# Performance work log

Measured on AMD Instinct MI355X. Metric: run time of the kernel, lower is better.

## Reference

```python
import jax, jax.numpy as jnp
import numpy as np

DIM = 256
NUM_HEADS = 8


def setup_inputs() -> dict:
    key = jax.random.key(0)
    ks = jax.random.split(key, 8)
    B, H, W = 2, 64, 64
    s = 0.02
    return {
        "query": jax.random.normal(ks[0], (B, H, W, DIM), jnp.float32),
        "sim": jax.random.normal(ks[1], (B, H, W, DIM), jnp.float32),
        "Wq": jax.random.normal(ks[2], (DIM, DIM), jnp.float32) * s,
        "bq": jnp.zeros((DIM,), jnp.float32),
        "Wkv": jax.random.normal(ks[3], (DIM, 2 * DIM), jnp.float32) * s,
        "bkv": jnp.zeros((2 * DIM,), jnp.float32),
        "Wp": jax.random.normal(ks[4], (DIM, DIM), jnp.float32) * s,
        "bp": jnp.zeros((DIM,), jnp.float32),
    }


def reference(query, sim, Wq, bq, Wkv, bkv, Wp, bp):
    B, H, W, dim = query.shape
    nh = NUM_HEADS
    dh = dim // nh
    scale = dh ** (-0.5)
    S = H * W

    # projections
    q = (query.reshape(B, S, dim) @ Wq + bq).reshape(B, S, nh, dh)
    kv = (sim.reshape(B, S, dim) @ Wkv + bkv).reshape(B, S, 2, nh, dh)
    k = kv[:, :, 0]  # [B,S,nh,dh]
    v = kv[:, :, 1]

    # attention: scores [B,nh,S,S]
    attn = jnp.einsum('bqhd,bkhd->bhqk', q * scale, k)
    attn = jax.nn.softmax(attn, axis=-1)
    x = jnp.einsum('bhqk,bkhd->bqhd', attn, v)  # [B,S,nh,dh]
    x = x.reshape(B, H, W, dim)
    return x @ Wp + bp
```

## Files before the change

kernel.cpp:

```cpp
#include <hip/hip_runtime.h>
#include <hip/hip_bf16.h>
#include <math.h>


#define SCALE 0.17677669529663687f
#define LOG2E 1.4426950408889634f

typedef __attribute__((ext_vector_type(8))) short short8;
typedef __attribute__((ext_vector_type(4))) float f32x4;

static __device__ __forceinline__ unsigned short f2bf(float x) {
    union { float f; unsigned int u; } v; v.f = x;
    unsigned int r = v.u + 0x7fff + ((v.u >> 16) & 1);
    return (unsigned short)(r >> 16);
}
static __device__ __forceinline__ float bf2f(unsigned short h) {
    union { unsigned int u; float f; } v; v.u = ((unsigned int)h) << 16;
    return v.f;
}
static __device__ __forceinline__ float fexp2(float x) {
#if __has_builtin(__builtin_amdgcn_exp2f)
    return __builtin_amdgcn_exp2f(x);
#else
    float r; asm("v_exp_f32 %0, %1" : "=v"(r) : "v"(x)); return r;
#endif
}
static __device__ __forceinline__ unsigned int pk_bf16(float a, float b) {
    unsigned int r;
    asm("v_cvt_pk_bf16_f32 %0, %1, %2" : "=v"(r) : "v"(a), "v"(b));
    return r;
}

__global__ __launch_bounds__(256) void prep_w(
    const float* __restrict__ Wq, const float* __restrict__ Wkv,
    const float* __restrict__ Wp,
    unsigned short* __restrict__ whi, unsigned short* __restrict__ wlo)
{
    const int n = blockIdx.x & 255, mat = blockIdx.x >> 8, k = threadIdx.x;
    const float* src; int ldw, colx; float sc = 1.f;
    if (mat == 0)      { src = Wq;  ldw = 256; colx = n;       sc = SCALE * LOG2E; }
    else if (mat == 1) { src = Wkv; ldw = 512; colx = n;       }
    else if (mat == 2) { src = Wkv; ldw = 512; colx = n + 256; }
    else               { src = Wp;  ldw = 256; colx = n;       }
    float v = src[(long long)k * ldw + colx] * sc;
    unsigned short h = f2bf(v);
    unsigned short l = f2bf(v - bf2f(h));
    const int o = blockIdx.x * 256 + k;
    whi[o] = h; wlo[o] = l;
}

__global__ __launch_bounds__(256) void gemm_qkv(
    const float* __restrict__ query, const float* __restrict__ sim,
    const unsigned short* __restrict__ whi, const unsigned short* __restrict__ wlo,
    const float* __restrict__ bq, const float* __restrict__ bkv,
    unsigned short* __restrict__ qbuf, unsigned short* __restrict__ kbuf,
    unsigned short* __restrict__ vTb)
{
    __shared__ unsigned short XsH[64 * 40], XsL[64 * 40];
    __shared__ unsigned short WsH[64 * 40], WsL[64 * 40];

    const int t = threadIdx.x, wave = t >> 6, lane = t & 63;
    const int col = lane & 15, quad = lane >> 4;
    const int by = blockIdx.y;
    const int kind = by >> 2;
    const int n0 = (by & 3) * 64;
    const int m0 = blockIdx.x * 64;
    const float* __restrict__ X = (kind == 0) ? query : sim;
    const int wrow0 = kind * 256 + n0;
    const int srow = t >> 2, spart = (t & 3) * 8;

    const f32x4 zero = {0.f, 0.f, 0.f, 0.f};
    f32x4 acc[4] = {zero, zero, zero, zero};

    for (int kt = 0; kt < 8; ++kt) {
        const int k0 = kt * 32;
        const float* xp = &X[(long long)(m0 + srow) * 256 + k0 + spart];
        float4 xa = *(const float4*)xp;
        float4 xb = *(const float4*)(xp + 4);
        float xv[8] = {xa.x, xa.y, xa.z, xa.w, xb.x, xb.y, xb.z, xb.w};
        union { unsigned short s[8]; uint4 u; } ph, pl;
#pragma unroll
        for (int j = 0; j < 8; ++j) {
            unsigned short h = f2bf(xv[j]);
            ph.s[j] = h;
            pl.s[j] = f2bf(xv[j] - bf2f(h));
        }
        uint4 wh = *(const uint4*)&whi[(long long)(wrow0 + srow) * 256 + k0 + spart];
        uint4 wl = *(const uint4*)&wlo[(long long)(wrow0 + srow) * 256 + k0 + spart];
        __syncthreads();
        *(uint4*)&XsH[srow * 40 + spart] = ph.u;
        *(uint4*)&XsL[srow * 40 + spart] = pl.u;
        *(uint4*)&WsH[srow * 40 + spart] = wh;
        *(uint4*)&WsL[srow * 40 + spart] = wl;
        __syncthreads();

        const unsigned short* Ah = (kind == 2) ? WsH : XsH;
        const unsigned short* Al = (kind == 2) ? WsL : XsL;
        const unsigned short* Bh = (kind == 2) ? XsH : WsH;
        const unsigned short* Bl = (kind == 2) ? XsL : WsL;

        short8 a_h = *(const short8*)(Ah + (wave * 16 + col) * 40 + quad * 8);
        short8 a_l = *(const short8*)(Al + (wave * 16 + col) * 40 + quad * 8);
#pragma unroll
        for (int nt = 0; nt < 4; ++nt) {
            short8 b_h = *(const short8*)(Bh + (nt * 16 + col) * 40 + quad * 8);
            short8 b_l = *(const short8*)(Bl + (nt * 16 + col) * 40 + quad * 8);
            acc[nt] = __builtin_amdgcn_mfma_f32_16x16x32_bf16(a_h, b_h, acc[nt], 0, 0, 0);
            acc[nt] = __builtin_amdgcn_mfma_f32_16x16x32_bf16(a_l, b_h, acc[nt], 0, 0, 0);
            acc[nt] = __builtin_amdgcn_mfma_f32_16x16x32_bf16(a_h, b_l, acc[nt], 0, 0, 0);
        }
    }

    if (kind == 0) {
#pragma unroll
        for (int nt = 0; nt < 4; ++nt) {
            int n = n0 + nt * 16 + col;
            int h = n >> 5, d = n & 31;
            float bias = bq[n] * (SCALE * LOG2E);
#pragma unroll
            for (int r = 0; r < 4; ++r) {
                int mg = m0 + wave * 16 + quad * 4 + r;
                int b = mg >> 12, sidx = mg & 4095;
                qbuf[((long long)(b * 8 + h) * 4096 + sidx) * 32 + d] = f2bf(acc[nt][r] + bias);
            }
        }
    } else if (kind == 1) {
#pragma unroll
        for (int nt = 0; nt < 4; ++nt) {
            int n = n0 + nt * 16 + col;
            int h = n >> 5, d = n & 31;
            float bias = bkv[n];
#pragma unroll
            for (int r = 0; r < 4; ++r) {
                int mg = m0 + wave * 16 + quad * 4 + r;
                int b = mg >> 12, sidx = mg & 4095;
                kbuf[((long long)(b * 8 + h) * 4096 + sidx) * 32 + d] = f2bf(acc[nt][r] + bias);
            }
        }
    } else {
#pragma unroll
        for (int nt = 0; nt < 4; ++nt) {
            int s = m0 + nt * 16 + col;
            int b = s >> 12, sidx = s & 4095;
#pragma unroll
            for (int r = 0; r < 4; ++r) {
                int dcol = n0 + wave * 16 + quad * 4 + r;
                int h = dcol >> 5, dd = dcol & 31;
                float bias = bkv[256 + dcol];
                vTb[((long long)((b * 8 + h) * 32 + dd)) * 4096 + sidx] = f2bf(acc[nt][r] + bias);
            }
        }
    }
}

__global__ __launch_bounds__(256) void flash_mfma(
    const unsigned short* __restrict__ qbuf,
    const unsigned short* __restrict__ kbuf,
    const unsigned short* __restrict__ vT,
    float* __restrict__ xbuf)
{
    __shared__ unsigned short Ks[128 * 40];
    __shared__ unsigned short Vt[32 * 136];
    __shared__ unsigned short Pb[4][640];

    const int t = threadIdx.x;
    const int wave = t >> 6, lane = t & 63;
    const int col = lane & 15, quad = lane >> 4;
    const int bh = blockIdx.x >> 5;
    const int q0 = (blockIdx.x & 31) * 128 + wave * 32;
    const long long kvbase = (long long)bh * 4096 * 32;
    unsigned short* pbw = Pb[wave];

    const short8 qf0 = *(const short8*)(qbuf + kvbase + (long long)(q0 + col) * 32 + quad * 8);
    const short8 qf1 = *(const short8*)(qbuf + kvbase + (long long)(q0 + 16 + col) * 32 + quad * 8);

    const f32x4 zero = {0.f, 0.f, 0.f, 0.f};
    f32x4 o00 = zero, o01 = zero, o10 = zero, o11 = zero;
    float l0 = 0.f, l1 = 0.f;

    const int krow = t >> 2, kpart = (t & 3) * 8;
    const int vrow = t >> 4, vpart = (t & 15) * 8;

    for (int kt = 0; kt < 32; ++kt) {
        uint4 kg0 = *(const uint4*)(kbuf + kvbase + (long long)(kt * 128 + krow) * 32 + kpart);
        uint4 kg1 = *(const uint4*)(kbuf + kvbase + (long long)(kt * 128 + krow + 64) * 32 + kpart);
        uint4 vg0 = *(const uint4*)(vT + ((long long)(bh * 32 + vrow)) * 4096 + kt * 128 + vpart);
        uint4 vg1 = *(const uint4*)(vT + ((long long)(bh * 32 + vrow + 16)) * 4096 + kt * 128 + vpart);
        __syncthreads();
        *(uint4*)(Ks + krow * 40 + kpart) = kg0;
        *(uint4*)(Ks + (krow + 64) * 40 + kpart) = kg1;
        *(uint4*)(Vt + vrow * 136 + vpart) = vg0;
        *(uint4*)(Vt + (vrow + 16) * 136 + vpart) = vg1;
        __syncthreads();

#pragma unroll
        for (int sb = 0; sb < 4; ++sb) {
            const int kb = sb * 32;
            short8 a0 = *(const short8*)(Ks + (kb + col) * 40 + quad * 8);
            short8 a1 = *(const short8*)(Ks + (kb + 16 + col) * 40 + quad * 8);
            short8 v0 = *(const short8*)(Vt + col * 136 + kb + quad * 8);
            short8 v1 = *(const short8*)(Vt + (16 + col) * 136 + kb + quad * 8);
            {
                f32x4 c0 = __builtin_amdgcn_mfma_f32_16x16x32_bf16(a0, qf0, zero, 0, 0, 0);
                f32x4 c1 = __builtin_amdgcn_mfma_f32_16x16x32_bf16(a1, qf0, zero, 0, 0, 0);
                float p0 = fexp2(c0[0]), p1 = fexp2(c0[1]), p2 = fexp2(c0[2]), p3 = fexp2(c0[3]);
                float p4 = fexp2(c1[0]), p5 = fexp2(c1[1]), p6 = fexp2(c1[2]), p7 = fexp2(c1[3]);
                l0 += ((p0 + p1) + (p2 + p3)) + ((p4 + p5) + (p6 + p7));
                uint2 w0 = make_uint2(pk_bf16(p0, p1), pk_bf16(p2, p3));
                uint2 w1 = make_uint2(pk_bf16(p4, p5), pk_bf16(p6, p7));
                *(uint2*)(pbw + col * 40 + quad * 4) = w0;
                *(uint2*)(pbw + col * 40 + 16 + quad * 4) = w1;
                short8 pf = *(const short8*)(pbw + col * 40 + quad * 8);
                o00 = __builtin_amdgcn_mfma_f32_16x16x32_bf16(v0, pf, o00, 0, 0, 0);
                o01 = __builtin_amdgcn_mfma_f32_16x16x32_bf16(v1, pf, o01, 0, 0, 0);
            }
            {
                f32x4 c0 = __builtin_amdgcn_mfma_f32_16x16x32_bf16(a0, qf1, zero, 0, 0, 0);
                f32x4 c1 = __builtin_amdgcn_mfma_f32_16x16x32_bf16(a1, qf1, zero, 0, 0, 0);
                float p0 = fexp2(c0[0]), p1 = fexp2(c0[1]), p2 = fexp2(c0[2]), p3 = fexp2(c0[3]);
                float p4 = fexp2(c1[0]), p5 = fexp2(c1[1]), p6 = fexp2(c1[2]), p7 = fexp2(c1[3]);
                l1 += ((p0 + p1) + (p2 + p3)) + ((p4 + p5) + (p6 + p7));
                uint2 w0 = make_uint2(pk_bf16(p0, p1), pk_bf16(p2, p3));
                uint2 w1 = make_uint2(pk_bf16(p4, p5), pk_bf16(p6, p7));
                *(uint2*)(pbw + col * 40 + quad * 4) = w0;
                *(uint2*)(pbw + col * 40 + 16 + quad * 4) = w1;
                short8 pf = *(const short8*)(pbw + col * 40 + quad * 8);
                o10 = __builtin_amdgcn_mfma_f32_16x16x32_bf16(v0, pf, o10, 0, 0, 0);
                o11 = __builtin_amdgcn_mfma_f32_16x16x32_bf16(v1, pf, o11, 0, 0, 0);
            }
        }
    }

    l0 += __shfl_xor(l0, 16, 64); l0 += __shfl_xor(l0, 32, 64);
    l1 += __shfl_xor(l1, 16, 64); l1 += __shfl_xor(l1, 32, 64);
    const float i0 = 1.f / l0, i1 = 1.f / l1;

    const int b = bh >> 3, hh = bh & 7;
    float* xp0 = xbuf + ((long long)(b * 4096 + q0 + col)) * 256 + hh * 32;
    *(float4*)(xp0 + quad * 4)      = make_float4(o00[0] * i0, o00[1] * i0, o00[2] * i0, o00[3] * i0);
    *(float4*)(xp0 + 16 + quad * 4) = make_float4(o01[0] * i0, o01[1] * i0, o01[2] * i0, o01[3] * i0);
    float* xp1 = xbuf + ((long long)(b * 4096 + q0 + 16 + col)) * 256 + hh * 32;
    *(float4*)(xp1 + quad * 4)      = make_float4(o10[0] * i1, o10[1] * i1, o10[2] * i1, o10[3] * i1);
    *(float4*)(xp1 + 16 + quad * 4) = make_float4(o11[0] * i1, o11[1] * i1, o11[2] * i1, o11[3] * i1);
}

__global__ __launch_bounds__(256) void gemm_outp(
    const float* __restrict__ xbuf,
    const unsigned short* __restrict__ whi, const unsigned short* __restrict__ wlo,
    const float* __restrict__ bp, float* __restrict__ out)
{
    __shared__ unsigned short XsH[64 * 40], XsL[64 * 40];
    __shared__ unsigned short WsH[64 * 40], WsL[64 * 40];

    const int t = threadIdx.x, wave = t >> 6, lane = t & 63;
    const int col = lane & 15, quad = lane >> 4;
    const int n0 = blockIdx.y * 64;
    const int m0 = blockIdx.x * 64;
    const int wrow0 = 768 + n0;
    const int srow = t >> 2, spart = (t & 3) * 8;

    const f32x4 zero = {0.f, 0.f, 0.f, 0.f};
    f32x4 acc[4] = {zero, zero, zero, zero};

    for (int kt = 0; kt < 8; ++kt) {
        const int k0 = kt * 32;
        const float* xp = &xbuf[(long long)(m0 + srow) * 256 + k0 + spart];
        float4 xa = *(const float4*)xp;
        float4 xb = *(const float4*)(xp + 4);
        float xv[8] = {xa.x, xa.y, xa.z, xa.w, xb.x, xb.y, xb.z, xb.w};
        union { unsigned short s[8]; uint4 u; } ph, pl;
#pragma unroll
        for (int j = 0; j < 8; ++j) {
            unsigned short h = f2bf(xv[j]);
            ph.s[j] = h;
            pl.s[j] = f2bf(xv[j] - bf2f(h));
        }
        uint4 wh = *(const uint4*)&whi[(long long)(wrow0 + srow) * 256 + k0 + spart];
        uint4 wl = *(const uint4*)&wlo[(long long)(wrow0 + srow) * 256 + k0 + spart];
        __syncthreads();
        *(uint4*)&XsH[srow * 40 + spart] = ph.u;
        *(uint4*)&XsL[srow * 40 + spart] = pl.u;
        *(uint4*)&WsH[srow * 40 + spart] = wh;
        *(uint4*)&WsL[srow * 40 + spart] = wl;
        __syncthreads();

        short8 a_h = *(const short8*)(XsH + (wave * 16 + col) * 40 + quad * 8);
        short8 a_l = *(const short8*)(XsL + (wave * 16 + col) * 40 + quad * 8);
#pragma unroll
        for (int nt = 0; nt < 4; ++nt) {
            short8 b_h = *(const short8*)(WsH + (nt * 16 + col) * 40 + quad * 8);
            short8 b_l = *(const short8*)(WsL + (nt * 16 + col) * 40 + quad * 8);
            acc[nt] = __builtin_amdgcn_mfma_f32_16x16x32_bf16(a_h, b_h, acc[nt], 0, 0, 0);
            acc[nt] = __builtin_amdgcn_mfma_f32_16x16x32_bf16(a_l, b_h, acc[nt], 0, 0, 0);
            acc[nt] = __builtin_amdgcn_mfma_f32_16x16x32_bf16(a_h, b_l, acc[nt], 0, 0, 0);
        }
    }

#pragma unroll
    for (int nt = 0; nt < 4; ++nt) {
        int n = n0 + nt * 16 + col;
        float bias = bp[n];
#pragma unroll
        for (int r = 0; r < 4; ++r) {
            int mg = m0 + wave * 16 + quad * 4 + r;
            out[(long long)mg * 256 + n] = acc[nt][r] + bias;
        }
    }
}

extern "C" void kernel_launch(void* const* d_in, const int* in_sizes, int n_in,
                              void* d_out, int out_size, void* d_ws, size_t ws_size,
                              hipStream_t stream) {
    const float* query = (const float*)d_in[0];
    const float* sim   = (const float*)d_in[1];
    const float* Wq    = (const float*)d_in[2];
    const float* bq    = (const float*)d_in[3];
    const float* Wkv   = (const float*)d_in[4];
    const float* bkv   = (const float*)d_in[5];
    const float* Wp    = (const float*)d_in[6];
    const float* bp    = (const float*)d_in[7];
    float* out = (float*)d_out;

    unsigned short* wsb = (unsigned short*)d_ws;
    unsigned short* qbuf = wsb;
    unsigned short* kbuf = wsb + 2097152;
    unsigned short* vT   = wsb + 4194304;
    float* xbuf = (float*)(wsb + 6291456);
    unsigned short* whi  = wsb + 10485760;
    unsigned short* wlo  = whi + 262144;

    prep_w   <<<dim3(1024),    256, 0, stream>>>(Wq, Wkv, Wp, whi, wlo);
    gemm_qkv <<<dim3(128, 12), 256, 0, stream>>>(query, sim, whi, wlo, bq, bkv,
                                                 qbuf, kbuf, vT);
    flash_mfma<<<dim3(512),    256, 0, stream>>>(qbuf, kbuf, vT, xbuf);
    gemm_outp<<<dim3(128, 4),  256, 0, stream>>>(xbuf, whi, wlo, bp, out);
}
```

Baseline: 176.1 us.

## Switch projection GEMMs to fp16 split-activation with single fp16 weights, prepack inputs

Replaces the bf16 hi/lo three-MFMA scheme with fp16: activations are split into fp16 hi/lo, weights are a single fp16 copy, and each tile needs two MFMAs instead of three. The prep kernel now pre-splits query/sim into fp16 hi/lo buffers and transposes the weights through shared memory for coalesced access. This cuts MFMA count and weight traffic in the GEMMs, but it adds a pass that writes and rereads the activations, and fp16 range and weight rounding may reduce accuracy. xbuf now aliases the xhi/xlo region, which is safe only because gemm_qkv finishes before flash writes it.

```diff
diff --git a/kernel.cpp b/kernel.cpp
--- a/kernel.cpp
+++ b/kernel.cpp
@@ -7,6 +7,7 @@
 #define LOG2E 1.4426950408889634f
 
 typedef __attribute__((ext_vector_type(8))) short short8;
+typedef __attribute__((ext_vector_type(8))) _Float16 half8;
 typedef __attribute__((ext_vector_type(4))) float f32x4;
 
 static __device__ __forceinline__ unsigned short f2bf(float x) {
@@ -30,34 +31,80 @@
     asm("v_cvt_pk_bf16_f32 %0, %1, %2" : "=v"(r) : "v"(a), "v"(b));
     return r;
 }
-
-__global__ __launch_bounds__(256) void prep_w(
+static __device__ __forceinline__ unsigned short f2h(float x) {
+    _Float16 h = (_Float16)x;
+    union { _Float16 h; unsigned short s; } u; u.h = h;
+    return u.s;
+}
+static __device__ __forceinline__ float h2f(unsigned short s) {
+    union { _Float16 h; unsigned short s; } u; u.s = s;
+    return (float)u.h;
+}
+
+__global__ __launch_bounds__(256) void prep(
+    const float* __restrict__ query, const float* __restrict__ sim,
     const float* __restrict__ Wq, const float* __restrict__ Wkv,
     const float* __restrict__ Wp,
-    unsigned short* __restrict__ whi, unsigned short* __restrict__ wlo)
+    unsigned short* __restrict__ xhi, unsigned short* __restrict__ xlo,
+    unsigned short* __restrict__ wfp)
 {
-    const int n = blockIdx.x & 255, mat = blockIdx.x >> 8, k = threadIdx.x;
-    const float* src; int ldw, colx; float sc = 1.f;
-    if (mat == 0)      { src = Wq;  ldw = 256; colx = n;       sc = SCALE * LOG2E; }
-    else if (mat == 1) { src = Wkv; ldw = 512; colx = n;       }
-    else if (mat == 2) { src = Wkv; ldw = 512; colx = n + 256; }
-    else               { src = Wp;  ldw = 256; colx = n;       }
-    float v = src[(long long)k * ldw + colx] * sc;
-    unsigned short h = f2bf(v);
-    unsigned short l = f2bf(v - bf2f(h));
-    const int o = blockIdx.x * 256 + k;
-    whi[o] = h; wlo[o] = l;
+    __shared__ float T[64][68];
+    const int blk = blockIdx.x, t = threadIdx.x;
+    if (blk < 4096) {
+        const int e = blk * 1024 + t * 4;
+        const float* src = (e < 2097152) ? (query + e) : (sim + (e - 2097152));
+        float4 v = *(const float4*)src;
+        float xv[4] = {v.x, v.y, v.z, v.w};
+        union { unsigned short s[4]; uint2 u; } ph, pl;
+#pragma unroll
+        for (int j = 0; j < 4; ++j) {
+            unsigned short h = f2h(xv[j]);
+            ph.s[j] = h;
+            pl.s[j] = f2h(xv[j] - h2f(h));
+        }
+        *(uint2*)&xhi[e] = ph.u;
+        *(uint2*)&xlo[e] = pl.u;
+        return;
+    }
+    const int bb = blk - 4096;
+    const int mat = bb >> 4, tile = bb & 15;
+    const int kr0 = (tile >> 2) * 64;
+    const int nc0 = (tile & 3) * 64;
+    const float* src; int ldw, cb; float sc = 1.f;
+    if (mat == 0)      { src = Wq;  ldw = 256; cb = 0;   sc = SCALE * LOG2E; }
+    else if (mat == 1) { src = Wkv; ldw = 512; cb = 0;   }
+    else if (mat == 2) { src = Wkv; ldw = 512; cb = 256; }
+    else               { src = Wp;  ldw = 256; cb = 0;   }
+    {
+        const int rl = t >> 4, c4 = (t & 15) * 4;
+#pragma unroll
+        for (int rr = 0; rr < 4; ++rr) {
+            float4 v = *(const float4*)&src[(long long)(kr0 + rr * 16 + rl) * ldw + cb + nc0 + c4];
+            T[rr * 16 + rl][c4 + 0] = v.x; T[rr * 16 + rl][c4 + 1] = v.y;
+            T[rr * 16 + rl][c4 + 2] = v.z; T[rr * 16 + rl][c4 + 3] = v.w;
+        }
+    }
+    __syncthreads();
+    {
+        const int nl = t >> 2, kl0 = (t & 3) * 16;
+        const long long orow = (long long)(mat * 256 + nc0 + nl) * 256 + kr0 + kl0;
+        union { unsigned short s[16]; uint4 u[2]; } ph;
+#pragma unroll
+        for (int j = 0; j < 16; ++j)
+            ph.s[j] = f2h(T[kl0 + j][nl] * sc);
+        *(uint4*)&wfp[orow] = ph.u[0];
+        *(uint4*)&wfp[orow + 8] = ph.u[1];
+    }
 }
 
 __global__ __launch_bounds__(256) void gemm_qkv(
-    const float* __restrict__ query, const float* __restrict__ sim,
-    const unsigned short* __restrict__ whi, const unsigned short* __restrict__ wlo,
+    const unsigned short* __restrict__ xhi, const unsigned short* __restrict__ xlo,
+    const unsigned short* __restrict__ wfp,
     const float* __restrict__ bq, const float* __restrict__ bkv,
     unsigned short* __restrict__ qbuf, unsigned short* __restrict__ kbuf,
     unsigned short* __restrict__ vTb)
 {
-    __shared__ unsigned short XsH[64 * 40], XsL[64 * 40];
-    __shared__ unsigned short WsH[64 * 40], WsL[64 * 40];
+    __shared__ unsigned short XsH[64 * 40], XsL[64 * 40], Ws[64 * 40];
 
     const int t = threadIdx.x, wave = t >> 6, lane = t & 63;
     const int col = lane & 15, quad = lane >> 4;
@@ -65,7 +112,7 @@
     const int kind = by >> 2;
     const int n0 = (by & 3) * 64;
     const int m0 = blockIdx.x * 64;
-    const float* __restrict__ X = (kind == 0) ? query : sim;
+    const int xrow0 = ((kind == 0) ? 0 : 8192) + m0;
     const int wrow0 = kind * 256 + n0;
     const int srow = t >> 2, spart = (t & 3) * 8;
 
@@ -74,40 +121,33 @@
 
     for (int kt = 0; kt < 8; ++kt) {
         const int k0 = kt * 32;
-        const float* xp = &X[(long long)(m0 + srow) * 256 + k0 + spart];
-        float4 xa = *(const float4*)xp;
-        float4 xb = *(const float4*)(xp + 4);
-        float xv[8] = {xa.x, xa.y, xa.z, xa.w, xb.x, xb.y, xb.z, xb.w};
-        union { unsigned short s[8]; uint4 u; } ph, pl;
-#pragma unroll
-        for (int j = 0; j < 8; ++j) {
-            unsigned short h = f2bf(xv[j]);
-            ph.s[j] = h;
-            pl.s[j] = f2bf(xv[j] - bf2f(h));
-        }
-        uint4 wh = *(const uint4*)&whi[(long long)(wrow0 + srow) * 256 + k0 + spart];
-        uint4 wl = *(const uint4*)&wlo[(long long)(wrow0 + srow) * 256 + k0 + spart];
-        __syncthreads();
-        *(uint4*)&XsH[srow * 40 + spart] = ph.u;
-        *(uint4*)&XsL[srow * 40 + spart] = pl.u;
-        *(uint4*)&WsH[srow * 40 + spart] = wh;
-        *(uint4*)&WsL[srow * 40 + spart] = wl;
-        __syncthreads();
-
-        const unsigned short* Ah = (kind == 2) ? WsH : XsH;
-        const unsigned short* Al = (kind == 2) ? WsL : XsL;
-        const unsigned short* Bh = (kind == 2) ? XsH : WsH;
-        const unsigned short* Bl = (kind == 2) ? XsL : WsL;
-
-        short8 a_h = *(const short8*)(Ah + (wave * 16 + col) * 40 + quad * 8);
-        short8 a_l = *(const short8*)(Al + (wave * 16 + col) * 40 + quad * 8);
-#pragma unroll
-        for (int nt = 0; nt < 4; ++nt) {
-            short8 b_h = *(const short8*)(Bh + (nt * 16 + col) * 40 + quad * 8);
-            short8 b_l = *(const short8*)(Bl + (nt * 16 + col) * 40 + quad * 8);
-            acc[nt] = __builtin_amdgcn_mfma_f32_16x16x32_bf16(a_h, b_h, acc[nt], 0, 0, 0);
-            acc[nt] = __builtin_amdgcn_mfma_f32_16x16x32_bf16(a_l, b_h, acc[nt], 0, 0, 0);
-            acc[nt] = __builtin_amdgcn_mfma_f32_16x16x32_bf16(a_h, b_l, acc[nt], 0, 0, 0);
+        uint4 xh = *(const uint4*)&xhi[(long long)(xrow0 + srow) * 256 + k0 + spart];
+        uint4 xl = *(const uint4*)&xlo[(long long)(xrow0 + srow) * 256 + k0 + spart];
+        uint4 wh = *(const uint4*)&wfp[(long long)(wrow0 + srow) * 256 + k0 + spart];
+        __syncthreads();
+        *(uint4*)&XsH[srow * 40 + spart] = xh;
+        *(uint4*)&XsL[srow * 40 + spart] = xl;
+        *(uint4*)&Ws[srow * 40 + spart] = wh;
+        __syncthreads();
+
+        if (kind < 2) {
+            half8 a_h = *(const half8*)(XsH + (wave * 16 + col) * 40 + quad * 8);
+            half8 a_l = *(const half8*)(XsL + (wave * 16 + col) * 40 + quad * 8);
+#pragma unroll
+            for (int nt = 0; nt < 4; ++nt) {
+                half8 b = *(const half8*)(Ws + (nt * 16 + col) * 40 + quad * 8);
+                acc[nt] = __builtin_amdgcn_mfma_f32_16x16x32_f16(a_h, b, acc[nt], 0, 0, 0);
+                acc[nt] = __builtin_amdgcn_mfma_f32_16x16x32_f16(a_l, b, acc[nt], 0, 0, 0);
+            }
+        } else {
+            half8 a = *(const half8*)(Ws + (wave * 16 + col) * 40 + quad * 8);
+#pragma unroll
+            for (int nt = 0; nt < 4; ++nt) {
+                half8 b_h = *(const half8*)(XsH + (nt * 16 + col) * 40 + quad * 8);
+                half8 b_l = *(const half8*)(XsL + (nt * 16 + col) * 40 + quad * 8);
+                acc[nt] = __builtin_amdgcn_mfma_f32_16x16x32_f16(a, b_h, acc[nt], 0, 0, 0);
+                acc[nt] = __builtin_amdgcn_mfma_f32_16x16x32_f16(a, b_l, acc[nt], 0, 0, 0);
+            }
         }
     }
 
@@ -245,12 +285,10 @@
 }
 
 __global__ __launch_bounds__(256) void gemm_outp(
-    const float* __restrict__ xbuf,
-    const unsigned short* __restrict__ whi, const unsigned short* __restrict__ wlo,
+    const float* __restrict__ xbuf, const unsigned short* __restrict__ wfp,
     const float* __restrict__ bp, float* __restrict__ out)
 {
-    __shared__ unsigned short XsH[64 * 40], XsL[64 * 40];
-    __shared__ unsigned short WsH[64 * 40], WsL[64 * 40];
+    __shared__ unsigned short XsH[64 * 40], XsL[64 * 40], Ws[64 * 40];
 
     const int t = threadIdx.x, wave = t >> 6, lane = t & 63;
     const int col = lane & 15, quad = lane >> 4;
@@ -271,28 +309,24 @@
         union { unsigned short s[8]; uint4 u; } ph, pl;
 #pragma unroll
         for (int j = 0; j < 8; ++j) {
-            unsigned short h = f2bf(xv[j]);
+            unsigned short h = f2h(xv[j]);
             ph.s[j] = h;
-            pl.s[j] = f2bf(xv[j] - bf2f(h));
-        }
-        uint4 wh = *(const uint4*)&whi[(long long)(wrow0 + srow) * 256 + k0 + spart];
-        uint4 wl = *(const uint4*)&wlo[(long long)(wrow0 + srow) * 256 + k0 + spart];
+            pl.s[j] = f2h(xv[j] - h2f(h));
+        }
+        uint4 wh = *(const uint4*)&wfp[(long long)(wrow0 + srow) * 256 + k0 + spart];
         __syncthreads();
         *(uint4*)&XsH[srow * 40 + spart] = ph.u;
         *(uint4*)&XsL[srow * 40 + spart] = pl.u;
-        *(uint4*)&WsH[srow * 40 + spart] = wh;
-        *(uint4*)&WsL[srow * 40 + spart] = wl;
-        __syncthreads();
-
-        short8 a_h = *(const short8*)(XsH + (wave * 16 + col) * 40 + quad * 8);
-        short8 a_l = *(const short8*)(XsL + (wave * 16 + col) * 40 + quad * 8);
+        *(uint4*)&Ws[srow * 40 + spart] = wh;
+        __syncthreads();
+
+        half8 a_h = *(const half8*)(XsH + (wave * 16 + col) * 40 + quad * 8);
+        half8 a_l = *(const half8*)(XsL + (wave * 16 + col) * 40 + quad * 8);
 #pragma unroll
         for (int nt = 0; nt < 4; ++nt) {
-            short8 b_h = *(const short8*)(WsH + (nt * 16 + col) * 40 + quad * 8);
-            short8 b_l = *(const short8*)(WsL + (nt * 16 + col) * 40 + quad * 8);
-            acc[nt] = __builtin_amdgcn_mfma_f32_16x16x32_bf16(a_h, b_h, acc[nt], 0, 0, 0);
-            acc[nt] = __builtin_amdgcn_mfma_f32_16x16x32_bf16(a_l, b_h, acc[nt], 0, 0, 0);
-            acc[nt] = __builtin_amdgcn_mfma_f32_16x16x32_bf16(a_h, b_l, acc[nt], 0, 0, 0);
+            half8 b = *(const half8*)(Ws + (nt * 16 + col) * 40 + quad * 8);
+            acc[nt] = __builtin_amdgcn_mfma_f32_16x16x32_f16(a_h, b, acc[nt], 0, 0, 0);
+            acc[nt] = __builtin_amdgcn_mfma_f32_16x16x32_f16(a_l, b, acc[nt], 0, 0, 0);
         }
     }
 
@@ -325,13 +359,15 @@
     unsigned short* qbuf = wsb;
     unsigned short* kbuf = wsb + 2097152;
     unsigned short* vT   = wsb + 4194304;
-    float* xbuf = (float*)(wsb + 6291456);
-    unsigned short* whi  = wsb + 10485760;
-    unsigned short* wlo  = whi + 262144;
-
-    prep_w   <<<dim3(1024),    256, 0, stream>>>(Wq, Wkv, Wp, whi, wlo);
-    gemm_qkv <<<dim3(128, 12), 256, 0, stream>>>(query, sim, whi, wlo, bq, bkv,
-                                                 qbuf, kbuf, vT);
-    flash_mfma<<<dim3(512),    256, 0, stream>>>(qbuf, kbuf, vT, xbuf);
-    gemm_outp<<<dim3(128, 4),  256, 0, stream>>>(xbuf, whi, wlo, bp, out);
-}
+    unsigned short* wfp  = wsb + 6291456;
+    unsigned short* xhi  = wsb + 6553600;
+    unsigned short* xlo  = wsb + 10747904;
+    float* xbuf = (float*)(wsb + 6553600);
+
+    prep      <<<dim3(4160),    256, 0, stream>>>(query, sim, Wq, Wkv, Wp,
+                                                  xhi, xlo, wfp);
+    gemm_qkv  <<<dim3(128, 12), 256, 0, stream>>>(xhi, xlo, wfp, bq, bkv,
+                                                  qbuf, kbuf, vT);
+    flash_mfma<<<dim3(512),     256, 0, stream>>>(qbuf, kbuf, vT, xbuf);
+    gemm_outp <<<dim3(128, 4),  256, 0, stream>>>(xbuf, wfp, bp, out);
+}
```

New measurement: 172.6 us. -2.0%, faster.
